# Kernel optimization log

Hardware: AMD Instinct MI355X
Metric: run time of the kernel (lower is better)

The kernel has to match this reference:

```python
import jax, jax.numpy as jnp
import numpy as np

_SAMPLING_EPS = 1e-5
_NEG_INF = jnp.float32(-jnp.inf)


def setup_inputs() -> dict:
    key = jax.random.key(0)
    k0, k1, k2, k3, k4, k5 = jax.random.split(key, 6)
    T, B, D, V = 4096, 64, 2048, 128000
    hidden_states = jax.random.normal(k0, (T, D), jnp.float32)
    embedding = jax.random.normal(k1, (V, D), jnp.float32) * 0.02
    last_token_indices = jnp.sort(jax.random.randint(k2, (B,), 0, T)).astype(jnp.int64)
    temperatures = jax.random.uniform(k3, (B,), jnp.float32, 0.1, 1.5)
    top_ps = jax.random.uniform(k4, (B,), jnp.float32, 0.5, 1.0)
    top_ks = jax.random.randint(k5, (B,), 1, 1024).astype(jnp.int64)
    return {
        "hidden_states": hidden_states,
        "embedding": embedding,
        "last_token_indices": last_token_indices,
        "temperatures": temperatures,
        "top_ps": top_ps,
        "top_ks": top_ks,
    }


def reference(hidden_states, embedding, last_token_indices, temperatures, top_ps, top_ks):
    V = embedding.shape[0]
    # 1) prune: keep last token of each sequence -> [B, D]
    h = hidden_states[last_token_indices]
    # 2) logits = h @ E^T -> [B, V]
    logits = jnp.einsum("bd,vd->bv", h, embedding)
    # 3) temperature scaling (temp < eps treated as 1.0, greedy handled below)
    t = jnp.where(temperatures < _SAMPLING_EPS, 1.0, temperatures)
    logits = logits / t[:, None]
    # 4) batched top-k in sorted (descending) domain
    sorted_idx = jnp.argsort(-logits, axis=-1)                      # [B, V]
    sorted_logits = jnp.take_along_axis(logits, sorted_idx, axis=-1)
    k = jnp.clip(top_ks, 1, V)
    keep_topk = jnp.arange(V)[None, :] < k[:, None]                  # [B, V]
    sorted_logits = jnp.where(keep_topk, sorted_logits, _NEG_INF)
    # 5) top-p (nucleus) on top-k-filtered, sorted logits
    sorted_probs = jax.nn.softmax(sorted_logits, axis=-1)
    cum = jnp.cumsum(sorted_probs, axis=-1)
    mask_p = (cum > top_ps[:, None]) & (top_ps[:, None] < 1.0 - _SAMPLING_EPS)
    mask_p = mask_p.at[:, 0].set(False)  # always keep the top token
    sorted_logits = jnp.where(mask_p, _NEG_INF, sorted_logits)
    # 6) scatter back to original vocab order
    inv_idx = jnp.argsort(sorted_idx, axis=-1)
    final_logits = jnp.take_along_axis(sorted_logits, inv_idx, axis=-1)
    probs = jax.nn.softmax(final_logits, axis=-1)
    # 7) multinomial sampling via Gumbel-max trick (deterministic key)
    u = jax.random.uniform(jax.random.key(42), probs.shape, jnp.float32, 1e-20, 1.0)
    gumbel = -jnp.log(-jnp.log(u))
    sampled = jnp.argmax(final_logits + gumbel, axis=-1)
    # 8) greedy path when temperature ~ 0
    greedy = jnp.argmax(logits, axis=-1)
    token_ids = jnp.where(temperatures < _SAMPLING_EPS, greedy, sampled)
    # sanitize (clamp out-of-range to 0)
    token_ids = jnp.where((token_ids < 0) | (token_ids >= V), 0, token_ids)
    return token_ids.astype(jnp.int64), probs
```

## Files before the change

kernel.cpp:

```cpp
#include <hip/hip_runtime.h>
#include <hip/hip_bf16.h>
#include <math.h>

#define CAP 2048
#define PRNG_PARTITIONABLE 1

typedef __attribute__((ext_vector_type(8))) short bf16x8;
typedef __attribute__((ext_vector_type(4))) float f32x4;
typedef __attribute__((ext_vector_type(4))) unsigned int u32x4;

union B8U4 { u32x4 u; bf16x8 b; };

__device__ __forceinline__ unsigned int f2ord(float x) {
  unsigned int u = __float_as_uint(x);
  return (u & 0x80000000u) ? ~u : (u | 0x80000000u);
}

__device__ __forceinline__ unsigned int rotl_u32(unsigned int x, int r) {
  return (x << r) | (x >> (32 - r));
}

__device__ float gumbel_at(unsigned int flat, unsigned int half_n) {
  const unsigned int ks0 = 0u;
  const unsigned int ks1 = 42u;
  const unsigned int ks2 = 0x1BD11BDAu ^ ks0 ^ ks1;
  unsigned int x0, x1;
#if PRNG_PARTITIONABLE
  x0 = 0u;
  x1 = flat;
#else
  unsigned int cnt = (flat < half_n) ? flat : (flat - half_n);
  x0 = cnt; x1 = cnt + half_n;
#endif
  x0 += ks0; x1 += ks1;
#define TF_R(r) { x0 += x1; x1 = rotl_u32(x1, r); x1 ^= x0; }
  TF_R(13) TF_R(15) TF_R(26) TF_R(6)
  x0 += ks1; x1 += ks2 + 1u;
  TF_R(17) TF_R(29) TF_R(16) TF_R(24)
  x0 += ks2; x1 += ks0 + 2u;
  TF_R(13) TF_R(15) TF_R(26) TF_R(6)
  x0 += ks0; x1 += ks1 + 3u;
  TF_R(17) TF_R(29) TF_R(16) TF_R(24)
  x0 += ks1; x1 += ks2 + 4u;
  TF_R(13) TF_R(15) TF_R(26) TF_R(6)
  x0 += ks2; x1 += ks0 + 5u;
#undef TF_R
#if PRNG_PARTITIONABLE
  unsigned int bits = x0 ^ x1;
#else
  unsigned int bits = (flat < half_n) ? x0 : x1;
#endif
  float f = __uint_as_float(0x3f800000u | (bits >> 9)) - 1.0f;
  float u = fmaxf(1e-20f, f + 1e-20f);
  return -logf(-logf(u));
}

__device__ __forceinline__ unsigned short f32_to_bf16_rne(float x) {
  unsigned int u = __float_as_uint(x);
  unsigned int r = u + 0x7fffu + ((u >> 16) & 1u);
  return (unsigned short)(r >> 16);
}
__device__ __forceinline__ float bf16u_to_f32(unsigned short h) {
  return __uint_as_float(((unsigned int)h) << 16);
}

struct HL { unsigned int h, l; };
__device__ __forceinline__ HL cvt_pair(float a, float b) {
  float2 xf = make_float2(a, b);
  __hip_bfloat162 hh = __float22bfloat162_rn(xf);
  float2 hf = __bfloat1622float2(hh);
  __hip_bfloat162 ll = __float22bfloat162_rn(make_float2(a - hf.x, b - hf.y));
  HL r;
  __builtin_memcpy(&r.h, &hh, 4);
  __builtin_memcpy(&r.l, &ll, 4);
  return r;
}

__device__ __forceinline__ f32x4 mfma16(bf16x8 a, bf16x8 b, f32x4 c) {
  return __builtin_amdgcn_mfma_f32_16x16x32_bf16(a, b, c, 0, 0, 0);
}

__global__ void gather_split(const float* __restrict__ hidden, const int* __restrict__ lti,
                             unsigned short* __restrict__ Ah, unsigned short* __restrict__ Al,
                             int D) {
  int b = blockIdx.x;
  const float* src = hidden + (size_t)lti[b] * D;
  for (int i = threadIdx.x; i < D; i += blockDim.x) {
    float x = src[i];
    unsigned short h = f32_to_bf16_rne(x);
    float r = x - bf16u_to_f32(h);
    Ah[(size_t)b * D + i] = h;
    Al[(size_t)b * D + i] = f32_to_bf16_rne(r);
  }
}

#define BN 128
#define BK 64
__global__ __launch_bounds__(256) void gemm_mfma(
    const unsigned short* __restrict__ Ahg, const unsigned short* __restrict__ Alg,
    const float* __restrict__ E, float* __restrict__ outL, int D, int V) {
  __shared__ __align__(16) float BS[128 * 64];
  __shared__ __align__(16) unsigned short AhS[64 * 64];
  __shared__ __align__(16) unsigned short AlS[64 * 64];

  const int t = threadIdx.x;
  const int lane = t & 63;
  const int wv = t >> 6;
  const long n0 = (long)blockIdx.x * BN;
  const int am = t >> 2, ao = t & 3;

  f32x4 acc[4][2];
#pragma unroll
  for (int i = 0; i < 4; ++i)
#pragma unroll
    for (int j = 0; j < 2; ++j) acc[i][j] = (f32x4){0.f, 0.f, 0.f, 0.f};

  f32x4 bA[8], bB[8];
  bf16x8 aA[4], aB[4];

  auto LOAD = [&](f32x4* br, bf16x8* ar, int k0) {
#pragma unroll
    for (int q = 0; q < 4; ++q) {
      int gi = q * 256 + t, n = gi >> 3, o = gi & 7;
      const float* s = E + (size_t)(n0 + n) * D + k0 + o * 8;
      br[2 * q] = *(const f32x4*)s;
      br[2 * q + 1] = *(const f32x4*)(s + 4);
    }
    const unsigned short* ph = Ahg + (size_t)am * D + k0 + ao * 16;
    ar[0] = *(const bf16x8*)ph;
    ar[1] = *(const bf16x8*)(ph + 8);
    const unsigned short* pl = Alg + (size_t)am * D + k0 + ao * 16;
    ar[2] = *(const bf16x8*)pl;
    ar[3] = *(const bf16x8*)(pl + 8);
  };

  auto STAGE = [&](f32x4* br, bf16x8* ar) {
#pragma unroll
    for (int q = 0; q < 4; ++q) {
      int gi = q * 256 + t, n = gi >> 3, o = gi & 7;
      int pg0 = (2 * o) ^ (n & 7);
      int pg1 = (2 * o + 1) ^ (n & 7);
      *(f32x4*)&BS[n * 64 + pg0 * 4] = br[2 * q];
      *(f32x4*)&BS[n * 64 + pg1 * 4] = br[2 * q + 1];
    }
    int g0 = ao * 2;
    int off0 = am * 64 + ((g0 ^ (am & 7)) * 8);
    int off1 = am * 64 + (((g0 + 1) ^ (am & 7)) * 8);
    *(bf16x8*)&AhS[off0] = ar[0];
    *(bf16x8*)&AhS[off1] = ar[1];
    *(bf16x8*)&AlS[off0] = ar[2];
    *(bf16x8*)&AlS[off1] = ar[3];
  };

  auto COMPUTE = [&]() {
#pragma unroll
    for (int k32 = 0; k32 < 2; ++k32) {
      const int og = k32 * 4 + (lane >> 4);
      bf16x8 ah[4], al[4], bh[2], bl[2];
#pragma unroll
      for (int mf = 0; mf < 4; ++mf) {
        int r = mf * 16 + (lane & 15);
        int off = r * 64 + ((og ^ (r & 7)) * 8);
        ah[mf] = *(const bf16x8*)&AhS[off];
        al[mf] = *(const bf16x8*)&AlS[off];
      }
#pragma unroll
      for (int nf = 0; nf < 2; ++nf) {
        int n = wv * 32 + nf * 16 + (lane & 15);
        int pg0 = (2 * og) ^ (n & 7);
        int pg1 = (2 * og + 1) ^ (n & 7);
        f32x4 v0 = *(const f32x4*)&BS[n * 64 + pg0 * 4];
        f32x4 v1 = *(const f32x4*)&BS[n * 64 + pg1 * 4];
        HL p0 = cvt_pair(v0.x, v0.y);
        HL p1 = cvt_pair(v0.z, v0.w);
        HL p2 = cvt_pair(v1.x, v1.y);
        HL p3 = cvt_pair(v1.z, v1.w);
        B8U4 hb, lb;
        hb.u = (u32x4){p0.h, p1.h, p2.h, p3.h};
        lb.u = (u32x4){p0.l, p1.l, p2.l, p3.l};
        bh[nf] = hb.b;
        bl[nf] = lb.b;
      }
      __builtin_amdgcn_s_setprio(1);
#pragma unroll
      for (int mf = 0; mf < 4; ++mf)
#pragma unroll
        for (int nf = 0; nf < 2; ++nf) {
          acc[mf][nf] = mfma16(ah[mf], bh[nf], acc[mf][nf]);
          acc[mf][nf] = mfma16(ah[mf], bl[nf], acc[mf][nf]);
          acc[mf][nf] = mfma16(al[mf], bh[nf], acc[mf][nf]);
        }
      __builtin_amdgcn_s_setprio(0);
    }
  };

  LOAD(bA, aA, 0);
#pragma unroll 1
  for (int k0 = 0; k0 < D; k0 += 2 * BK) {
    if (k0 + BK < D) LOAD(bB, aB, k0 + BK);
    __syncthreads();
    STAGE(bA, aA);
    __syncthreads();
    COMPUTE();
    if (k0 + 2 * BK < D) LOAD(bA, aA, k0 + 2 * BK);
    __syncthreads();
    STAGE(bB, aB);
    __syncthreads();
    COMPUTE();
  }

#pragma unroll
  for (int mf = 0; mf < 4; ++mf)
#pragma unroll
    for (int nf = 0; nf < 2; ++nf) {
      long v = n0 + wv * 32 + nf * 16 + (lane & 15);
      int rbase = mf * 16 + ((lane >> 4) << 2);
#pragma unroll
      for (int reg = 0; reg < 4; ++reg)
        outL[(size_t)(rbase + reg) * V + v] = acc[mf][nf][reg];
    }
}

__global__ __launch_bounds__(256) void hist_k(
    const float* __restrict__ logits, unsigned int* __restrict__ ghist, int V) {
  const int b = blockIdx.x >> 3, c = blockIdx.x & 7;
  const int CH = V >> 3;
  const float* row = logits + (size_t)b * V;
  __shared__ unsigned int lh[4][256];
  const int tid = threadIdx.x, wv = tid >> 6;
  for (int i = tid; i < 1024; i += 256) ((unsigned int*)lh)[i] = 0u;
  __syncthreads();
  const int base = c * CH;
  for (int i = base + tid * 4; i < base + CH; i += 1024) {
    f32x4 v = *(const f32x4*)(row + i);
    atomicAdd(&lh[wv][f2ord(v.x) >> 24], 1u);
    atomicAdd(&lh[wv][f2ord(v.y) >> 24], 1u);
    atomicAdd(&lh[wv][f2ord(v.z) >> 24], 1u);
    atomicAdd(&lh[wv][f2ord(v.w) >> 24], 1u);
  }
  __syncthreads();
  if (tid < 256) {
    unsigned int s = lh[0][tid] + lh[1][tid] + lh[2][tid] + lh[3][tid];
    if (s) atomicAdd(&ghist[b * 256 + tid], s);
  }
}

__global__ __launch_bounds__(256) void thresh1_k(
    const unsigned int* __restrict__ ghist, const int* __restrict__ top_ks,
    unsigned int* __restrict__ tau16, int* __restrict__ bin_b,
    int* __restrict__ need_b, int* __restrict__ refine_b, int V) {
  const int b = blockIdx.x, tid = threadIdx.x;
  __shared__ unsigned int h[256];
  if (tid < 256) h[tid] = ghist[b * 256 + tid];
  __syncthreads();
  if (tid == 0) {
    int k = top_ks[b];
    if (k < 1) k = 1;
    if (k > V) k = V;
    unsigned int run = 0;
    int bin = 255;
    for (; bin >= 0; --bin) {
      unsigned int hh = h[bin];
      if (run + hh >= (unsigned int)k) break;
      run += hh;
    }
    if (bin < 0) bin = 0;
    int refine = (run + h[bin] > (unsigned int)CAP) ? 1 : 0;
    bin_b[b] = bin;
    need_b[b] = k - (int)run;
    refine_b[b] = refine;
    if (!refine) tau16[b] = ((unsigned int)bin) << 8;
  }
}

__global__ __launch_bounds__(256) void refine_k(
    const float* __restrict__ logits, const int* __restrict__ bin_b,
    const int* __restrict__ refine_b, unsigned int* __restrict__ ghist2, int V) {
  const int b = blockIdx.x >> 3, c = blockIdx.x & 7;
  if (!refine_b[b]) return;
  const int CH = V >> 3;
  const float* row = logits + (size_t)b * V;
  __shared__ unsigned int lh[4][256];
  const int tid = threadIdx.x, wv = tid >> 6;
  for (int i = tid; i < 1024; i += 256) ((unsigned int*)lh)[i] = 0u;
  __syncthreads();
  const unsigned int binq = (unsigned int)bin_b[b];
  const int base = c * CH;
  for (int i = base + tid * 4; i < base + CH; i += 1024) {
    f32x4 v = *(const f32x4*)(row + i);
#pragma unroll
    for (int e = 0; e < 4; ++e) {
      unsigned int u = f2ord(v[e]);
      if ((u >> 24) == binq) atomicAdd(&lh[wv][(u >> 16) & 255u], 1u);
    }
  }
  __syncthreads();
  if (tid < 256) {
    unsigned int s = lh[0][tid] + lh[1][tid] + lh[2][tid] + lh[3][tid];
    if (s) atomicAdd(&ghist2[b * 256 + tid], s);
  }
}

__global__ __launch_bounds__(256) void thresh2_k(
    const unsigned int* __restrict__ ghist2, const int* __restrict__ bin_b,
    const int* __restrict__ need_b, const int* __restrict__ refine_b,
    unsigned int* __restrict__ tau16) {
  const int b = blockIdx.x, tid = threadIdx.x;
  if (!refine_b[b]) return;
  __shared__ unsigned int h[256];
  if (tid < 256) h[tid] = ghist2[b * 256 + tid];
  __syncthreads();
  if (tid == 0) {
    int need = need_b[b];
    unsigned int run = 0;
    int sub = 255;
    for (; sub >= 0; --sub) {
      unsigned int hh = h[sub];
      if (run + hh >= (unsigned int)need) break;
      run += hh;
    }
    if (sub < 0) sub = 0;
    tau16[b] = (((unsigned int)bin_b[b]) << 8) | (unsigned int)sub;
  }
}

__global__ __launch_bounds__(256) void gather_k(
    float* __restrict__ logits, const unsigned int* __restrict__ tau16,
    float* __restrict__ cvals, int* __restrict__ cidx, int* __restrict__ ccnt, int V) {
  const int b = blockIdx.x >> 3, c = blockIdx.x & 7;
  const int CH = V >> 3;
  float* row = logits + (size_t)b * V;
  __shared__ float bv[CAP];
  __shared__ int bi[CAP];
  __shared__ int s_c, s_base;
  const int tid = threadIdx.x;
  if (tid == 0) s_c = 0;
  __syncthreads();
  const unsigned int tau = tau16[b];
  const int base = c * CH;
  const f32x4 z = (f32x4){0.f, 0.f, 0.f, 0.f};
  for (int i = base + tid * 4; i < base + CH; i += 1024) {
    f32x4 v = *(const f32x4*)(row + i);
#pragma unroll
    for (int e = 0; e < 4; ++e) {
      float x = v[e];
      if ((f2ord(x) >> 16) >= tau) {
        int p = atomicAdd(&s_c, 1);
        if (p < CAP) { bv[p] = x; bi[p] = i + e; }
      }
    }
    *(f32x4*)(row + i) = z;
  }
  __syncthreads();
  int cnt = s_c;
  if (cnt > CAP) cnt = CAP;
  if (tid == 0) s_base = atomicAdd(ccnt + b, cnt);
  __syncthreads();
  const int gb = s_base;
  for (int i = tid; i < cnt; i += 256) {
    int p = gb + i;
    if (p < CAP) {
      cvals[(size_t)b * CAP + p] = bv[i];
      cidx[(size_t)b * CAP + p] = bi[i];
    }
  }
}

__global__ __launch_bounds__(1024) void finalize_k(
    const float* __restrict__ cvals, const int* __restrict__ cidx,
    const int* __restrict__ ccnt, const int* __restrict__ top_ks,
    const float* __restrict__ temps, const float* __restrict__ top_ps,
    float* __restrict__ out, int probs_base, int V, unsigned int half_n) {
  const int b = blockIdx.x, tid = threadIdx.x;
  __shared__ float vals[CAP];
  __shared__ int idxs[CAP];
  __shared__ float ex[1024];
  __shared__ float pr[1024];
  __shared__ float rsc[1024];
  __shared__ int rid[1024];
  __shared__ float s_S, s_S2;
  __shared__ int s_m;

  int cnt = ccnt[b];
  if (cnt > CAP) cnt = CAP;
  int k = top_ks[b];
  if (k < 1) k = 1;
  if (k > V) k = V;
  int K = (k < cnt) ? k : cnt;
  if (K > 1024) K = 1024;

  for (int i = tid; i < CAP; i += 1024) {
    if (i < cnt) { vals[i] = cvals[(size_t)b * CAP + i]; idxs[i] = cidx[(size_t)b * CAP + i]; }
    else         { vals[i] = -INFINITY;                  idxs[i] = 0x7fffffff; }
  }
  __syncthreads();

  for (int size = 2; size <= CAP; size <<= 1) {
    for (int stride = size >> 1; stride > 0; stride >>= 1) {
      for (int i = tid; i < CAP; i += 1024) {
        int j = i ^ stride;
        if (j > i) {
          float vi = vals[i], vj = vals[j];
          int ii = idxs[i], ij = idxs[j];
          bool iBeforeJ = (vi > vj) || (vi == vj && ii < ij);
          bool up = ((i & size) == 0);
          if (up ? !iBeforeJ : iBeforeJ) {
            vals[i] = vj; idxs[i] = ij; vals[j] = vi; idxs[j] = ii;
          }
        }
      }
      __syncthreads();
    }
  }

  const float t = temps[b];
  const float tt = (t < 1e-5f) ? 1.0f : t;
  const float l0 = vals[0] / tt;
  for (int i = tid; i < 1024; i += 1024) {
    ex[i] = (i < K) ? expf(vals[i] / tt - l0) : 0.f;
  }
  __syncthreads();

  rsc[tid] = ex[tid];
  __syncthreads();
  for (int s = 512; s > 0; s >>= 1) {
    if (tid < s) rsc[tid] += rsc[tid + s];
    __syncthreads();
  }
  if (tid == 0) s_S = rsc[0];
  __syncthreads();
  const float S = s_S;

  const float p = top_ps[b];
  int m;
  if (p >= 1.0f - 1e-5f) {
    m = K;
  } else {
    pr[tid] = ex[tid] / S;
    __syncthreads();
    for (int off = 1; off < 1024; off <<= 1) {
      float v = pr[tid] + ((tid >= off) ? pr[tid - off] : 0.f);
      __syncthreads();
      pr[tid] = v;
      __syncthreads();
    }
    rid[tid] = (tid < K && pr[tid] <= p) ? 1 : 0;
    __syncthreads();
    for (int s = 512; s > 0; s >>= 1) {
      if (tid < s) rid[tid] += rid[tid + s];
      __syncthreads();
    }
    if (tid == 0) s_m = (rid[0] < 1) ? 1 : rid[0];
    __syncthreads();
    m = s_m;
  }
  __syncthreads();

  rsc[tid] = (tid < m) ? ex[tid] : 0.f;
  __syncthreads();
  for (int s = 512; s > 0; s >>= 1) {
    if (tid < s) rsc[tid] += rsc[tid + s];
    __syncthreads();
  }
  if (tid == 0) s_S2 = rsc[0];
  __syncthreads();
  const float S2 = s_S2;

  for (int i = tid; i < m; i += 1024)
    out[(size_t)probs_base + (size_t)b * V + idxs[i]] = ex[i] / S2;

  float best = -INFINITY;
  int bestV = 0x7fffffff;
  for (int i = tid; i < m; i += 1024) {
    int vv = idxs[i];
    unsigned int flat = (unsigned int)b * (unsigned int)V + (unsigned int)vv;
    float g = gumbel_at(flat, half_n);
    float sc = vals[i] / tt + g;
    if (sc > best || (sc == best && vv < bestV)) { best = sc; bestV = vv; }
  }
  rsc[tid] = best; rid[tid] = bestV;
  __syncthreads();
  for (int s = 512; s > 0; s >>= 1) {
    if (tid < s) {
      float o = rsc[tid + s]; int oi = rid[tid + s];
      if (o > rsc[tid] || (o == rsc[tid] && oi < rid[tid])) { rsc[tid] = o; rid[tid] = oi; }
    }
    __syncthreads();
  }
  if (tid == 0) {
    int token = (t < 1e-5f) ? idxs[0] : rid[0];
    if (token < 0 || token >= V) token = 0;
    out[b] = (float)token;
  }
}

extern "C" void kernel_launch(void* const* d_in, const int* in_sizes, int n_in,
                              void* d_out, int out_size, void* d_ws, size_t ws_size,
                              hipStream_t stream) {
  const float* hidden = (const float*)d_in[0];
  const float* emb    = (const float*)d_in[1];
  const int*   lti    = (const int*)d_in[2];
  const float* temps  = (const float*)d_in[3];
  const float* tops   = (const float*)d_in[4];
  const int*   topks  = (const int*)d_in[5];

  const int B = in_sizes[2];
  const int V = (int)(((long long)out_size - B) / B);
  const int D = in_sizes[1] / V;
  const int probs_base = out_size - B * V;
  const unsigned int half_n = (unsigned int)(((long long)B * V) / 2);

  float* out = (float*)d_out;

  char* ws = (char*)d_ws;
  size_t off = 0;
  unsigned short* Ah = (unsigned short*)(ws + off); off += (size_t)B * D * sizeof(unsigned short);
  unsigned short* Al = (unsigned short*)(ws + off); off += (size_t)B * D * sizeof(unsigned short);
  float* cvals = (float*)(ws + off); off += (size_t)B * CAP * sizeof(float);
  int* cidx = (int*)(ws + off);      off += (size_t)B * CAP * sizeof(int);
  char* zbase = ws + off;
  int* ccnt = (int*)(ws + off);                    off += (size_t)B * sizeof(int);
  unsigned int* ghist = (unsigned int*)(ws + off); off += (size_t)B * 256 * sizeof(unsigned int);
  unsigned int* ghist2 = (unsigned int*)(ws + off); off += (size_t)B * 256 * sizeof(unsigned int);
  const size_t zbytes = (size_t)(B + B * 256 + B * 256) * sizeof(unsigned int);
  unsigned int* tau16 = (unsigned int*)(ws + off); off += (size_t)B * sizeof(unsigned int);
  int* bin_b = (int*)(ws + off);                   off += (size_t)B * sizeof(int);
  int* need_b = (int*)(ws + off);                  off += (size_t)B * sizeof(int);
  int* refine_b = (int*)(ws + off);                off += (size_t)B * sizeof(int);
  (void)ws_size; (void)n_in;

  float* logits = out + probs_base;

  hipLaunchKernelGGL(gather_split, dim3(B), dim3(256), 0, stream, hidden, lti, Ah, Al, D);
  hipMemsetAsync(zbase, 0, zbytes, stream);
  hipLaunchKernelGGL(gemm_mfma, dim3(V / BN), dim3(256), 0, stream, Ah, Al, emb, logits, D, V);
  hipLaunchKernelGGL(hist_k, dim3(8 * B), dim3(256), 0, stream, logits, ghist, V);
  hipLaunchKernelGGL(thresh1_k, dim3(B), dim3(256), 0, stream, ghist, topks, tau16, bin_b, need_b, refine_b, V);
  hipLaunchKernelGGL(refine_k, dim3(8 * B), dim3(256), 0, stream, logits, bin_b, refine_b, ghist2, V);
  hipLaunchKernelGGL(thresh2_k, dim3(B), dim3(256), 0, stream, ghist2, bin_b, need_b, refine_b, tau16);
  hipLaunchKernelGGL(gather_k, dim3(8 * B), dim3(256), 0, stream, logits, tau16, cvals, cidx, ccnt, V);
  hipLaunchKernelGGL(finalize_k, dim3(B), dim3(1024), 0, stream, cvals, cidx, ccnt,
                     topks, temps, tops, out, probs_base, V, half_n);
}
```

Measured before the change: 348.5 us.

## Use 12-bit radix histogram and merge threshold/refine kernels into one

The first-pass histogram widens from 256 to 4096 bins using the top 12 bits of the order-preserving key, and one 1024-thread threshold kernel replaces the thresh1/refine/thresh2 chain. That kernel finds the cutoff bin with a parallel suffix scan. Only when the candidate count would exceed CAP does it run a single-block refine pass over the row. This removes two kernel launches and the usual full 8-way refine pass, at the cost of a larger per-block shared histogram, more global atomics in hist_k, and a serial single-block refine in the rare overflow case.

New measurement: 328.3 us. 5.8% less time.

```diff
diff --git a/kernel.cpp b/kernel.cpp
--- a/kernel.cpp
+++ b/kernel.cpp
@@ -226,106 +226,104 @@
   const int b = blockIdx.x >> 3, c = blockIdx.x & 7;
   const int CH = V >> 3;
   const float* row = logits + (size_t)b * V;
-  __shared__ unsigned int lh[4][256];
-  const int tid = threadIdx.x, wv = tid >> 6;
-  for (int i = tid; i < 1024; i += 256) ((unsigned int*)lh)[i] = 0u;
+  __shared__ unsigned int lh[4096];
+  const int tid = threadIdx.x;
+  for (int i = tid; i < 4096; i += 256) lh[i] = 0u;
   __syncthreads();
   const int base = c * CH;
   for (int i = base + tid * 4; i < base + CH; i += 1024) {
     f32x4 v = *(const f32x4*)(row + i);
-    atomicAdd(&lh[wv][f2ord(v.x) >> 24], 1u);
-    atomicAdd(&lh[wv][f2ord(v.y) >> 24], 1u);
-    atomicAdd(&lh[wv][f2ord(v.z) >> 24], 1u);
-    atomicAdd(&lh[wv][f2ord(v.w) >> 24], 1u);
-  }
-  __syncthreads();
-  if (tid < 256) {
-    unsigned int s = lh[0][tid] + lh[1][tid] + lh[2][tid] + lh[3][tid];
-    if (s) atomicAdd(&ghist[b * 256 + tid], s);
-  }
-}
-
-__global__ __launch_bounds__(256) void thresh1_k(
-    const unsigned int* __restrict__ ghist, const int* __restrict__ top_ks,
-    unsigned int* __restrict__ tau16, int* __restrict__ bin_b,
-    int* __restrict__ need_b, int* __restrict__ refine_b, int V) {
+    atomicAdd(&lh[f2ord(v.x) >> 20], 1u);
+    atomicAdd(&lh[f2ord(v.y) >> 20], 1u);
+    atomicAdd(&lh[f2ord(v.z) >> 20], 1u);
+    atomicAdd(&lh[f2ord(v.w) >> 20], 1u);
+  }
+  __syncthreads();
+  for (int i = tid; i < 4096; i += 256) {
+    unsigned int s = lh[i];
+    if (s) atomicAdd(&ghist[(size_t)b * 4096 + i], s);
+  }
+}
+
+__global__ __launch_bounds__(1024) void thresh_k(
+    const float* __restrict__ logits, const unsigned int* __restrict__ ghist,
+    const int* __restrict__ top_ks, unsigned int* __restrict__ tau20, int V) {
   const int b = blockIdx.x, tid = threadIdx.x;
-  __shared__ unsigned int h[256];
-  if (tid < 256) h[tid] = ghist[b * 256 + tid];
-  __syncthreads();
-  if (tid == 0) {
-    int k = top_ks[b];
-    if (k < 1) k = 1;
-    if (k > V) k = V;
-    unsigned int run = 0;
-    int bin = 255;
-    for (; bin >= 0; --bin) {
-      unsigned int hh = h[bin];
-      if (run + hh >= (unsigned int)k) break;
-      run += hh;
-    }
-    if (bin < 0) bin = 0;
-    int refine = (run + h[bin] > (unsigned int)CAP) ? 1 : 0;
-    bin_b[b] = bin;
-    need_b[b] = k - (int)run;
-    refine_b[b] = refine;
-    if (!refine) tau16[b] = ((unsigned int)bin) << 8;
-  }
-}
-
-__global__ __launch_bounds__(256) void refine_k(
-    const float* __restrict__ logits, const int* __restrict__ bin_b,
-    const int* __restrict__ refine_b, unsigned int* __restrict__ ghist2, int V) {
-  const int b = blockIdx.x >> 3, c = blockIdx.x & 7;
-  if (!refine_b[b]) return;
-  const int CH = V >> 3;
+  __shared__ unsigned int h[4096];
+  __shared__ unsigned int ts[1024];
+  __shared__ unsigned int h2[256];
+  __shared__ int s_bin, s_cntGT, s_found;
+
+  for (int i = tid; i < 4096; i += 1024) h[i] = ghist[(size_t)b * 4096 + i];
+  if (tid == 0) s_found = 0;
+  __syncthreads();
+
+  int k = top_ks[b];
+  if (k < 1) k = 1;
+  if (k > V) k = V;
+  const unsigned int uk = (unsigned int)k;
+
+  unsigned int s0 = h[4 * tid] + h[4 * tid + 1] + h[4 * tid + 2] + h[4 * tid + 3];
+  ts[tid] = s0;
+  __syncthreads();
+  for (int off = 1; off < 1024; off <<= 1) {
+    unsigned int v = ts[tid] + ((tid + off < 1024) ? ts[tid + off] : 0u);
+    __syncthreads();
+    ts[tid] = v;
+    __syncthreads();
+  }
+  unsigned int above = ts[tid] - s0;
+  if (above < uk && above + s0 >= uk) {
+    unsigned int run = above;
+    for (int j = 3; j >= 0; --j) {
+      unsigned int hj = h[4 * tid + j];
+      if (run < uk && run + hj >= uk) {
+        s_bin = 4 * tid + j;
+        s_cntGT = (int)run;
+        s_found = 1;
+        break;
+      }
+      run += hj;
+    }
+  }
+  __syncthreads();
+  int bin = s_found ? s_bin : 0;
+  int cntGT = s_found ? s_cntGT : 0;
+
+  if (cntGT + (int)h[bin] <= CAP) {
+    if (tid == 0) tau20[b] = ((unsigned int)bin) << 8;
+    return;
+  }
+
+  for (int i = tid; i < 256; i += 1024) h2[i] = 0u;
+  __syncthreads();
   const float* row = logits + (size_t)b * V;
-  __shared__ unsigned int lh[4][256];
-  const int tid = threadIdx.x, wv = tid >> 6;
-  for (int i = tid; i < 1024; i += 256) ((unsigned int*)lh)[i] = 0u;
-  __syncthreads();
-  const unsigned int binq = (unsigned int)bin_b[b];
-  const int base = c * CH;
-  for (int i = base + tid * 4; i < base + CH; i += 1024) {
+  const unsigned int binq = (unsigned int)bin;
+  for (int i = tid * 4; i < V; i += 4096) {
     f32x4 v = *(const f32x4*)(row + i);
 #pragma unroll
     for (int e = 0; e < 4; ++e) {
       unsigned int u = f2ord(v[e]);
-      if ((u >> 24) == binq) atomicAdd(&lh[wv][(u >> 16) & 255u], 1u);
-    }
-  }
-  __syncthreads();
-  if (tid < 256) {
-    unsigned int s = lh[0][tid] + lh[1][tid] + lh[2][tid] + lh[3][tid];
-    if (s) atomicAdd(&ghist2[b * 256 + tid], s);
-  }
-}
-
-__global__ __launch_bounds__(256) void thresh2_k(
-    const unsigned int* __restrict__ ghist2, const int* __restrict__ bin_b,
-    const int* __restrict__ need_b, const int* __restrict__ refine_b,
-    unsigned int* __restrict__ tau16) {
-  const int b = blockIdx.x, tid = threadIdx.x;
-  if (!refine_b[b]) return;
-  __shared__ unsigned int h[256];
-  if (tid < 256) h[tid] = ghist2[b * 256 + tid];
+      if ((u >> 20) == binq) atomicAdd(&h2[(u >> 12) & 255u], 1u);
+    }
+  }
   __syncthreads();
   if (tid == 0) {
-    int need = need_b[b];
+    int need = k - cntGT;
     unsigned int run = 0;
     int sub = 255;
     for (; sub >= 0; --sub) {
-      unsigned int hh = h[sub];
+      unsigned int hh = h2[sub];
       if (run + hh >= (unsigned int)need) break;
       run += hh;
     }
     if (sub < 0) sub = 0;
-    tau16[b] = (((unsigned int)bin_b[b]) << 8) | (unsigned int)sub;
+    tau20[b] = (binq << 8) | (unsigned int)sub;
   }
 }
 
 __global__ __launch_bounds__(256) void gather_k(
-    float* __restrict__ logits, const unsigned int* __restrict__ tau16,
+    float* __restrict__ logits, const unsigned int* __restrict__ tau20,
     float* __restrict__ cvals, int* __restrict__ cidx, int* __restrict__ ccnt, int V) {
   const int b = blockIdx.x >> 3, c = blockIdx.x & 7;
   const int CH = V >> 3;
@@ -336,7 +334,7 @@
   const int tid = threadIdx.x;
   if (tid == 0) s_c = 0;
   __syncthreads();
-  const unsigned int tau = tau16[b];
+  const unsigned int tau = tau20[b];
   const int base = c * CH;
   const f32x4 z = (f32x4){0.f, 0.f, 0.f, 0.f};
   for (int i = base + tid * 4; i < base + CH; i += 1024) {
@@ -344,7 +342,7 @@
 #pragma unroll
     for (int e = 0; e < 4; ++e) {
       float x = v[e];
-      if ((f2ord(x) >> 16) >= tau) {
+      if ((f2ord(x) >> 12) >= tau) {
         int p = atomicAdd(&s_c, 1);
         if (p < CAP) { bv[p] = x; bi[p] = i + e; }
       }
@@ -416,9 +414,7 @@
   const float t = temps[b];
   const float tt = (t < 1e-5f) ? 1.0f : t;
   const float l0 = vals[0] / tt;
-  for (int i = tid; i < 1024; i += 1024) {
-    ex[i] = (i < K) ? expf(vals[i] / tt - l0) : 0.f;
-  }
+  ex[tid] = (tid < K) ? expf(vals[tid] / tt - l0) : 0.f;
   __syncthreads();
 
   rsc[tid] = ex[tid];
@@ -520,13 +516,9 @@
   int* cidx = (int*)(ws + off);      off += (size_t)B * CAP * sizeof(int);
   char* zbase = ws + off;
   int* ccnt = (int*)(ws + off);                    off += (size_t)B * sizeof(int);
-  unsigned int* ghist = (unsigned int*)(ws + off); off += (size_t)B * 256 * sizeof(unsigned int);
-  unsigned int* ghist2 = (unsigned int*)(ws + off); off += (size_t)B * 256 * sizeof(unsigned int);
-  const size_t zbytes = (size_t)(B + B * 256 + B * 256) * sizeof(unsigned int);
-  unsigned int* tau16 = (unsigned int*)(ws + off); off += (size_t)B * sizeof(unsigned int);
-  int* bin_b = (int*)(ws + off);                   off += (size_t)B * sizeof(int);
-  int* need_b = (int*)(ws + off);                  off += (size_t)B * sizeof(int);
-  int* refine_b = (int*)(ws + off);                off += (size_t)B * sizeof(int);
+  unsigned int* ghist = (unsigned int*)(ws + off); off += (size_t)B * 4096 * sizeof(unsigned int);
+  const size_t zbytes = (size_t)(B + B * 4096) * sizeof(unsigned int);
+  unsigned int* tau20 = (unsigned int*)(ws + off); off += (size_t)B * sizeof(unsigned int);
   (void)ws_size; (void)n_in;
 
   float* logits = out + probs_base;
@@ -535,10 +527,8 @@
   hipMemsetAsync(zbase, 0, zbytes, stream);
   hipLaunchKernelGGL(gemm_mfma, dim3(V / BN), dim3(256), 0, stream, Ah, Al, emb, logits, D, V);
   hipLaunchKernelGGL(hist_k, dim3(8 * B), dim3(256), 0, stream, logits, ghist, V);
-  hipLaunchKernelGGL(thresh1_k, dim3(B), dim3(256), 0, stream, ghist, topks, tau16, bin_b, need_b, refine_b, V);
-  hipLaunchKernelGGL(refine_k, dim3(8 * B), dim3(256), 0, stream, logits, bin_b, refine_b, ghist2, V);
-  hipLaunchKernelGGL(thresh2_k, dim3(B), dim3(256), 0, stream, ghist2, bin_b, need_b, refine_b, tau16);
-  hipLaunchKernelGGL(gather_k, dim3(8 * B), dim3(256), 0, stream, logits, tau16, cvals, cidx, ccnt, V);
+  hipLaunchKernelGGL(thresh_k, dim3(B), dim3(1024), 0, stream, logits, ghist, topks, tau20, V);
+  hipLaunchKernelGGL(gather_k, dim3(8 * B), dim3(256), 0, stream, logits, tau20, cvals, cidx, ccnt, V);
   hipLaunchKernelGGL(finalize_k, dim3(B), dim3(1024), 0, stream, cvals, cidx, ccnt,
                      topks, temps, tops, out, probs_base, V, half_n);
 }
```
